# Kernel tuning notes

Measured on AMD Instinct MI355X. Metric: run time of the kernel, lower is better.

The kernel has to match this reference:

```python
import jax, jax.numpy as jnp
import numpy as np


def setup_inputs() -> dict:
    key = jax.random.key(0)
    bs, n_heads, ch, length = 4, 8, 64, 2048
    width = 3 * n_heads * ch  # 1536
    qkv = jax.random.normal(key, (bs, width, length), dtype=jnp.float32)
    return {"qkv": qkv, "n_heads": n_heads}


def reference(qkv, n_heads):
    bs, width, length = qkv.shape
    ch = width // (3 * n_heads)
    # reshape to (bs*heads, 3*ch, length) then split into q, k, v of (B, ch, L)
    qkv_r = qkv.reshape(bs * n_heads, 3 * ch, length)
    q, k, v = qkv_r[:, :ch], qkv_r[:, ch:2 * ch], qkv_r[:, 2 * ch:]
    scale = ch ** (-0.5)
    # weight = bmm(q^T, k) * scale -> (B, L_q, L_k)
    weight = jnp.einsum('bct,bcs->bts', q, k) * scale
    weight = jax.nn.softmax(weight.astype(jnp.float32), axis=-1).astype(qkv.dtype)
    # a = bmm(v, weight^T) -> (B, ch, L)
    a = jnp.einsum('bcs,bts->bct', v, weight)
    return a.reshape(bs, n_heads * ch, length)
```

## Files before the change

### kernel.cpp

```cpp
#include <hip/hip_runtime.h>

typedef __bf16 bf16;
typedef __attribute__((ext_vector_type(8)))  __bf16 bf16x8;
typedef __attribute__((ext_vector_type(16))) float  f32x16;

#define LEN   2048
#define CH    64
#define HEADS 32

union PackU { unsigned u[4]; bf16x8 v; };

static __device__ inline unsigned pack2(float lo, float hi) {
  union { bf16 h[2]; unsigned u; } p;
  p.h[0] = (bf16)lo; p.h[1] = (bf16)hi;
  return p.u;
}

static __device__ inline void async_cp16(const bf16* g, bf16* l) {
  __builtin_amdgcn_global_load_lds(
      (const __attribute__((address_space(1))) void*)g,
      (__attribute__((address_space(3))) void*)l, 16, 0, 0);
}

__global__ __launch_bounds__(256) void prep_kernel(const float* __restrict__ qkv,
                                                   bf16* __restrict__ ws) {
  __shared__ float tile[64][65];
  const int tIdx = blockIdx.x;
  const int g    = blockIdx.y;
  const int tid  = threadIdx.x;
  const int s0   = tIdx * 64;
  const float* K = qkv + (g * 192 + 64)  * LEN;
  const float* V = qkv + (g * 192 + 128) * LEN;

  {
    const int c0 = tid >> 6, s = tid & 63;
#pragma unroll
    for (int i = 0; i < 16; ++i) {
      const int c = c0 + i * 4;
      tile[c][s] = K[c * LEN + s0 + s];
    }
  }
  __syncthreads();

  bf16* dst = ws + ((size_t)g * 32 + tIdx) * 8192;
#pragma unroll
  for (int it = 0; it < 2; ++it) {
    const int c2  = tid + it * 256;
    const int row = c2 >> 3, cx = c2 & 7;
    const int cb  = (cx ^ (row & 7)) * 8;
    bf16x8 o;
#pragma unroll
    for (int j = 0; j < 8; ++j) o[j] = (bf16)tile[cb + j][row];
    *(bf16x8*)(dst + c2 * 8) = o;
  }
#pragma unroll
  for (int it = 0; it < 2; ++it) {
    const int c2  = tid + it * 256;
    const int row = c2 >> 3, cx = c2 & 7;
    const int k8  = cx ^ (row & 7);
    const int pa  = 32 * (k8 >> 2) + 8 * ((k8 >> 1) & 1) + 4 * (k8 & 1);
    const float* src = V + row * LEN + s0 + pa;
    const float4 a = *(const float4*)src;
    const float4 b = *(const float4*)(src + 16);
    bf16x8 o;
    o[0] = (bf16)a.x; o[1] = (bf16)a.y; o[2] = (bf16)a.z; o[3] = (bf16)a.w;
    o[4] = (bf16)b.x; o[5] = (bf16)b.y; o[6] = (bf16)b.z; o[7] = (bf16)b.w;
    *(bf16x8*)(dst + 4096 + c2 * 8) = o;
  }
}

__global__ __launch_bounds__(512, 2) void attn_kernel(const float* __restrict__ qkv,
                                                      const bf16* __restrict__ ws,
                                                      float* __restrict__ out) {
  __shared__ __align__(16) bf16 stg[32768];

  const int tid  = threadIdx.x;
  const int lane = tid & 63;
  const int w    = tid >> 6;
  const int wg   = w & 3;
  const int sg   = w >> 2;
  const int n    = lane & 31;
  const int h    = lane >> 5;
  const int g    = blockIdx.x & 31;
  const int jb   = blockIdx.x >> 5;
  const int t0   = jb * 256 + wg * 64;

  const bf16* wsg = ws + (size_t)g * (32 * 8192);

  auto stage = [&](int i) {
    const bf16* src = wsg + i * 8192;
    bf16* dst = stg + (i & 3) * 8192;
#pragma unroll
    for (int it = 0; it < 2; ++it) {
      const int chunk = w * 128 + it * 64 + lane;
      async_cp16(src + chunk * 8, dst + chunk * 8);
    }
  };
  stage(0); stage(1);

  const float qs = 0.125f * 1.44269504088896340736f;
  const float* Q = qkv + g * (192 * LEN);
  bf16x8 qf[2][4];
#pragma unroll
  for (int e = 0; e < 2; ++e)
#pragma unroll
    for (int kb = 0; kb < 4; ++kb)
#pragma unroll
      for (int jj = 0; jj < 8; ++jj)
        qf[e][kb][jj] = (bf16)(Q[(kb * 16 + h * 8 + jj) * LEN + t0 + e * 32 + n] * qs);

  f32x16 o_acc[2][2];
#pragma unroll
  for (int e = 0; e < 2; ++e)
#pragma unroll
    for (int mb = 0; mb < 2; ++mb)
#pragma unroll
      for (int r = 0; r < 16; ++r) o_acc[e][mb][r] = 0.f;
  float l_acc[2] = {0.f, 0.f};

  for (int p = 0; p < 16; ++p) {
    __syncthreads();
    if (p < 15) { stage(2 * p + 2); stage(2 * p + 3); }
    const bf16* ktl = stg + ((2 * p + sg) & 3) * 8192;
    const bf16* vl  = ktl + 4096;

    f32x16 sf[2][2];
#pragma unroll
    for (int e = 0; e < 2; ++e)
#pragma unroll
      for (int mb = 0; mb < 2; ++mb)
#pragma unroll
        for (int r = 0; r < 16; ++r) sf[e][mb][r] = 0.f;
#pragma unroll
    for (int kb = 0; kb < 4; ++kb)
#pragma unroll
      for (int mb = 0; mb < 2; ++mb) {
        const bf16x8 a = *(const bf16x8*)(ktl + (mb * 32 + n) * 64 + (((kb * 2 + h) ^ (n & 7)) * 8));
        sf[0][mb] = __builtin_amdgcn_mfma_f32_32x32x16_bf16(a, qf[0][kb], sf[0][mb], 0, 0, 0);
        sf[1][mb] = __builtin_amdgcn_mfma_f32_32x32x16_bf16(a, qf[1][kb], sf[1][mb], 0, 0, 0);
      }

    PackU frag[2][4];
#pragma unroll
    for (int e = 0; e < 2; ++e) {
      float ls = 0.f;
#pragma unroll
      for (int mb = 0; mb < 2; ++mb)
#pragma unroll
        for (int u = 0; u < 4; ++u) {
          const float p0 = __builtin_amdgcn_exp2f(sf[e][mb][4 * u + 0]);
          const float p1 = __builtin_amdgcn_exp2f(sf[e][mb][4 * u + 1]);
          const float p2 = __builtin_amdgcn_exp2f(sf[e][mb][4 * u + 2]);
          const float p3 = __builtin_amdgcn_exp2f(sf[e][mb][4 * u + 3]);
          ls += (p0 + p1) + (p2 + p3);
          const int kb   = 2 * mb + (u & 1);
          const int base = 2 * (u >> 1);
          frag[e][kb].u[base]     = pack2(p0, p1);
          frag[e][kb].u[base + 1] = pack2(p2, p3);
        }
      l_acc[e] += ls;
    }

#pragma unroll
    for (int kbs = 0; kbs < 4; ++kbs)
#pragma unroll
      for (int mbo = 0; mbo < 2; ++mbo) {
        const bf16x8 a = *(const bf16x8*)(vl + (mbo * 32 + n) * 64 + (((kbs * 2 + h) ^ (n & 7)) * 8));
        o_acc[0][mbo] = __builtin_amdgcn_mfma_f32_32x32x16_bf16(a, frag[0][kbs].v, o_acc[0][mbo], 0, 0, 0);
        o_acc[1][mbo] = __builtin_amdgcn_mfma_f32_32x32x16_bf16(a, frag[1][kbs].v, o_acc[1][mbo], 0, 0, 0);
      }
  }

  float lt[2];
#pragma unroll
  for (int e = 0; e < 2; ++e) lt[e] = l_acc[e] + __shfl_xor(l_acc[e], 32);

  float* fx = (float*)stg;
  float* lx = fx + 15104;

#pragma unroll
  for (int mbo = 0; mbo < 2; ++mbo) {
    __syncthreads();
    if (sg == 1) {
#pragma unroll
      for (int e = 0; e < 2; ++e)
#pragma unroll
        for (int u = 0; u < 4; ++u) {
          float4 st;
          st.x = o_acc[e][mbo][4 * u + 0];
          st.y = o_acc[e][mbo][4 * u + 1];
          st.z = o_acc[e][mbo][4 * u + 2];
          st.w = o_acc[e][mbo][4 * u + 3];
          *(float4*)&fx[wg * 2304 + (e * 32 + n) * 36 + 8 * u + 4 * h] = st;
        }
      if (mbo == 0 && h == 0) {
        lx[wg * 64 + n]      = lt[0];
        lx[wg * 64 + 32 + n] = lt[1];
      }
    }
    __syncthreads();
    if (sg == 0) {
#pragma unroll
      for (int e = 0; e < 2; ++e)
#pragma unroll
        for (int u = 0; u < 4; ++u) {
          const float4 q = *(const float4*)&fx[wg * 2304 + (e * 32 + n) * 36 + 8 * u + 4 * h];
          o_acc[e][mbo][4 * u + 0] += q.x;
          o_acc[e][mbo][4 * u + 1] += q.y;
          o_acc[e][mbo][4 * u + 2] += q.z;
          o_acc[e][mbo][4 * u + 3] += q.w;
        }
    }
  }

  if (sg == 0) {
    float inv[2];
#pragma unroll
    for (int e = 0; e < 2; ++e) inv[e] = 1.0f / (lt[e] + lx[wg * 64 + e * 32 + n]);
    float* og = out + g * (CH * LEN);
#pragma unroll
    for (int e = 0; e < 2; ++e)
#pragma unroll
      for (int mbo = 0; mbo < 2; ++mbo)
#pragma unroll
        for (int r = 0; r < 16; ++r) {
          const int c = 32 * mbo + (r & 3) + 8 * (r >> 2) + 4 * h;
          og[c * LEN + t0 + e * 32 + n] = o_acc[e][mbo][r] * inv[e];
        }
  }
}

extern "C" void kernel_launch(void* const* d_in, const int* in_sizes, int n_in,
                              void* d_out, int out_size, void* d_ws, size_t ws_size,
                              hipStream_t stream) {
  const float* qkv = (const float*)d_in[0];
  float* out = (float*)d_out;
  bf16* ws = (bf16*)d_ws;

  prep_kernel<<<dim3(32, HEADS), 256, 0, stream>>>(qkv, ws);
  attn_kernel<<<dim3(256), 512, 0, stream>>>(qkv, ws, out);
}
```

Baseline: 127.5 us.

## Halve per-wave query tile, double grid, and add extra LDS swizzle term

Each wave now handles one 32-column query group instead of two. The workgroup covers 128 queries instead of 256, so the grid doubles to 512 blocks and launch bounds are raised to allow 4 blocks per CU. A second XOR term on the row's upper bits is added to the K/V LDS swizzle, in both the prep kernel and the attention reads, to reduce bank conflicts. The intent is more parallelism and occupancy from fewer accumulator registers. In exchange, each block reloads the full K/V stream for fewer queries, doubling K/V staging traffic per query, and each 64 KB LDS buffer may cap residency below the requested count.

```diff
diff --git a/kernel.cpp b/kernel.cpp
--- a/kernel.cpp
+++ b/kernel.cpp
@@ -47,7 +47,8 @@
   for (int it = 0; it < 2; ++it) {
     const int c2  = tid + it * 256;
     const int row = c2 >> 3, cx = c2 & 7;
-    const int cb  = (cx ^ (row & 7)) * 8;
+    const int k8  = cx ^ (row & 7) ^ ((row >> 3) & 7);
+    const int cb  = k8 * 8;
     bf16x8 o;
 #pragma unroll
     for (int j = 0; j < 8; ++j) o[j] = (bf16)tile[cb + j][row];
@@ -57,7 +58,7 @@
   for (int it = 0; it < 2; ++it) {
     const int c2  = tid + it * 256;
     const int row = c2 >> 3, cx = c2 & 7;
-    const int k8  = cx ^ (row & 7);
+    const int k8  = cx ^ (row & 7) ^ ((row >> 3) & 7);
     const int pa  = 32 * (k8 >> 2) + 8 * ((k8 >> 1) & 1) + 4 * (k8 & 1);
     const float* src = V + row * LEN + s0 + pa;
     const float4 a = *(const float4*)src;
@@ -69,7 +70,7 @@
   }
 }
 
-__global__ __launch_bounds__(512, 2) void attn_kernel(const float* __restrict__ qkv,
+__global__ __launch_bounds__(512, 4) void attn_kernel(const float* __restrict__ qkv,
                                                       const bf16* __restrict__ ws,
                                                       float* __restrict__ out) {
   __shared__ __align__(16) bf16 stg[32768];
@@ -77,13 +78,14 @@
   const int tid  = threadIdx.x;
   const int lane = tid & 63;
   const int w    = tid >> 6;
-  const int wg   = w & 3;
+  const int wg   = w & 1;
+  const int eg   = (w >> 1) & 1;
   const int sg   = w >> 2;
   const int n    = lane & 31;
   const int h    = lane >> 5;
   const int g    = blockIdx.x & 31;
   const int jb   = blockIdx.x >> 5;
-  const int t0   = jb * 256 + wg * 64;
+  const int t0   = jb * 128 + wg * 64;
 
   const bf16* wsg = ws + (size_t)g * (32 * 8192);
 
@@ -100,23 +102,19 @@
 
   const float qs = 0.125f * 1.44269504088896340736f;
   const float* Q = qkv + g * (192 * LEN);
-  bf16x8 qf[2][4];
-#pragma unroll
-  for (int e = 0; e < 2; ++e)
-#pragma unroll
-    for (int kb = 0; kb < 4; ++kb)
-#pragma unroll
-      for (int jj = 0; jj < 8; ++jj)
-        qf[e][kb][jj] = (bf16)(Q[(kb * 16 + h * 8 + jj) * LEN + t0 + e * 32 + n] * qs);
-
-  f32x16 o_acc[2][2];
-#pragma unroll
-  for (int e = 0; e < 2; ++e)
-#pragma unroll
-    for (int mb = 0; mb < 2; ++mb)
-#pragma unroll
-      for (int r = 0; r < 16; ++r) o_acc[e][mb][r] = 0.f;
-  float l_acc[2] = {0.f, 0.f};
+  bf16x8 qf[4];
+#pragma unroll
+  for (int kb = 0; kb < 4; ++kb)
+#pragma unroll
+    for (int jj = 0; jj < 8; ++jj)
+      qf[kb][jj] = (bf16)(Q[(kb * 16 + h * 8 + jj) * LEN + t0 + eg * 32 + n] * qs);
+
+  f32x16 o_acc[2];
+#pragma unroll
+  for (int mb = 0; mb < 2; ++mb)
+#pragma unroll
+    for (int r = 0; r < 16; ++r) o_acc[mb][r] = 0.f;
+  float l_acc = 0.f;
 
   for (int p = 0; p < 16; ++p) {
     __syncthreads();
@@ -124,109 +122,91 @@
     const bf16* ktl = stg + ((2 * p + sg) & 3) * 8192;
     const bf16* vl  = ktl + 4096;
 
-    f32x16 sf[2][2];
-#pragma unroll
-    for (int e = 0; e < 2; ++e)
-#pragma unroll
-      for (int mb = 0; mb < 2; ++mb)
-#pragma unroll
-        for (int r = 0; r < 16; ++r) sf[e][mb][r] = 0.f;
+    f32x16 sf[2];
+#pragma unroll
+    for (int mb = 0; mb < 2; ++mb)
+#pragma unroll
+      for (int r = 0; r < 16; ++r) sf[mb][r] = 0.f;
 #pragma unroll
     for (int kb = 0; kb < 4; ++kb)
 #pragma unroll
       for (int mb = 0; mb < 2; ++mb) {
-        const bf16x8 a = *(const bf16x8*)(ktl + (mb * 32 + n) * 64 + (((kb * 2 + h) ^ (n & 7)) * 8));
-        sf[0][mb] = __builtin_amdgcn_mfma_f32_32x32x16_bf16(a, qf[0][kb], sf[0][mb], 0, 0, 0);
-        sf[1][mb] = __builtin_amdgcn_mfma_f32_32x32x16_bf16(a, qf[1][kb], sf[1][mb], 0, 0, 0);
-      }
-
-    PackU frag[2][4];
-#pragma unroll
-    for (int e = 0; e < 2; ++e) {
-      float ls = 0.f;
-#pragma unroll
-      for (int mb = 0; mb < 2; ++mb)
-#pragma unroll
-        for (int u = 0; u < 4; ++u) {
-          const float p0 = __builtin_amdgcn_exp2f(sf[e][mb][4 * u + 0]);
-          const float p1 = __builtin_amdgcn_exp2f(sf[e][mb][4 * u + 1]);
-          const float p2 = __builtin_amdgcn_exp2f(sf[e][mb][4 * u + 2]);
-          const float p3 = __builtin_amdgcn_exp2f(sf[e][mb][4 * u + 3]);
-          ls += (p0 + p1) + (p2 + p3);
-          const int kb   = 2 * mb + (u & 1);
-          const int base = 2 * (u >> 1);
-          frag[e][kb].u[base]     = pack2(p0, p1);
-          frag[e][kb].u[base + 1] = pack2(p2, p3);
-        }
-      l_acc[e] += ls;
-    }
+        const bf16x8 a = *(const bf16x8*)(ktl + (mb * 32 + n) * 64 +
+                          (((kb * 2 + h) ^ (n & 7) ^ (mb << 2) ^ (n >> 3)) * 8));
+        sf[mb] = __builtin_amdgcn_mfma_f32_32x32x16_bf16(a, qf[kb], sf[mb], 0, 0, 0);
+      }
+
+    PackU frag[4];
+    float ls = 0.f;
+#pragma unroll
+    for (int mb = 0; mb < 2; ++mb)
+#pragma unroll
+      for (int u = 0; u < 4; ++u) {
+        const float p0 = __builtin_amdgcn_exp2f(sf[mb][4 * u + 0]);
+        const float p1 = __builtin_amdgcn_exp2f(sf[mb][4 * u + 1]);
+        const float p2 = __builtin_amdgcn_exp2f(sf[mb][4 * u + 2]);
+        const float p3 = __builtin_amdgcn_exp2f(sf[mb][4 * u + 3]);
+        ls += (p0 + p1) + (p2 + p3);
+        const int kb   = 2 * mb + (u & 1);
+        const int base = 2 * (u >> 1);
+        frag[kb].u[base]     = pack2(p0, p1);
+        frag[kb].u[base + 1] = pack2(p2, p3);
+      }
+    l_acc += ls;
 
 #pragma unroll
     for (int kbs = 0; kbs < 4; ++kbs)
 #pragma unroll
       for (int mbo = 0; mbo < 2; ++mbo) {
-        const bf16x8 a = *(const bf16x8*)(vl + (mbo * 32 + n) * 64 + (((kbs * 2 + h) ^ (n & 7)) * 8));
-        o_acc[0][mbo] = __builtin_amdgcn_mfma_f32_32x32x16_bf16(a, frag[0][kbs].v, o_acc[0][mbo], 0, 0, 0);
-        o_acc[1][mbo] = __builtin_amdgcn_mfma_f32_32x32x16_bf16(a, frag[1][kbs].v, o_acc[1][mbo], 0, 0, 0);
-      }
-  }
-
-  float lt[2];
-#pragma unroll
-  for (int e = 0; e < 2; ++e) lt[e] = l_acc[e] + __shfl_xor(l_acc[e], 32);
+        const bf16x8 a = *(const bf16x8*)(vl + (mbo * 32 + n) * 64 +
+                          (((kbs * 2 + h) ^ (n & 7) ^ (mbo << 2) ^ (n >> 3)) * 8));
+        o_acc[mbo] = __builtin_amdgcn_mfma_f32_32x32x16_bf16(a, frag[kbs].v, o_acc[mbo], 0, 0, 0);
+      }
+  }
+
+  float lt = l_acc + __shfl_xor(l_acc, 32);
 
   float* fx = (float*)stg;
-  float* lx = fx + 15104;
+  float* lx = fx + 4608;
 
 #pragma unroll
   for (int mbo = 0; mbo < 2; ++mbo) {
     __syncthreads();
     if (sg == 1) {
 #pragma unroll
-      for (int e = 0; e < 2; ++e)
-#pragma unroll
-        for (int u = 0; u < 4; ++u) {
-          float4 st;
-          st.x = o_acc[e][mbo][4 * u + 0];
-          st.y = o_acc[e][mbo][4 * u + 1];
-          st.z = o_acc[e][mbo][4 * u + 2];
-          st.w = o_acc[e][mbo][4 * u + 3];
-          *(float4*)&fx[wg * 2304 + (e * 32 + n) * 36 + 8 * u + 4 * h] = st;
-        }
-      if (mbo == 0 && h == 0) {
-        lx[wg * 64 + n]      = lt[0];
-        lx[wg * 64 + 32 + n] = lt[1];
-      }
+      for (int u = 0; u < 4; ++u) {
+        float4 st;
+        st.x = o_acc[mbo][4 * u + 0];
+        st.y = o_acc[mbo][4 * u + 1];
+        st.z = o_acc[mbo][4 * u + 2];
+        st.w = o_acc[mbo][4 * u + 3];
+        *(float4*)&fx[wg * 2304 + (eg * 32 + n) * 36 + 8 * u + 4 * h] = st;
+      }
+      if (mbo == 0 && h == 0) lx[wg * 64 + eg * 32 + n] = lt;
     }
     __syncthreads();
     if (sg == 0) {
 #pragma unroll
-      for (int e = 0; e < 2; ++e)
-#pragma unroll
-        for (int u = 0; u < 4; ++u) {
-          const float4 q = *(const float4*)&fx[wg * 2304 + (e * 32 + n) * 36 + 8 * u + 4 * h];
-          o_acc[e][mbo][4 * u + 0] += q.x;
-          o_acc[e][mbo][4 * u + 1] += q.y;
-          o_acc[e][mbo][4 * u + 2] += q.z;
-          o_acc[e][mbo][4 * u + 3] += q.w;
-        }
+      for (int u = 0; u < 4; ++u) {
+        const float4 q = *(const float4*)&fx[wg * 2304 + (eg * 32 + n) * 36 + 8 * u + 4 * h];
+        o_acc[mbo][4 * u + 0] += q.x;
+        o_acc[mbo][4 * u + 1] += q.y;
+        o_acc[mbo][4 * u + 2] += q.z;
+        o_acc[mbo][4 * u + 3] += q.w;
+      }
     }
   }
 
   if (sg == 0) {
-    float inv[2];
-#pragma unroll
-    for (int e = 0; e < 2; ++e) inv[e] = 1.0f / (lt[e] + lx[wg * 64 + e * 32 + n]);
+    const float inv = 1.0f / (lt + lx[wg * 64 + eg * 32 + n]);
     float* og = out + g * (CH * LEN);
 #pragma unroll
-    for (int e = 0; e < 2; ++e)
-#pragma unroll
-      for (int mbo = 0; mbo < 2; ++mbo)
-#pragma unroll
-        for (int r = 0; r < 16; ++r) {
-          const int c = 32 * mbo + (r & 3) + 8 * (r >> 2) + 4 * h;
-          og[c * LEN + t0 + e * 32 + n] = o_acc[e][mbo][r] * inv[e];
-        }
+    for (int mbo = 0; mbo < 2; ++mbo)
+#pragma unroll
+      for (int r = 0; r < 16; ++r) {
+        const int c = 32 * mbo + (r & 3) + 8 * (r >> 2) + 4 * h;
+        og[c * LEN + t0 + eg * 32 + n] = o_acc[mbo][r] * inv;
+      }
   }
 }
 
@@ -238,5 +218,5 @@
   bf16* ws = (bf16*)d_ws;
 
   prep_kernel<<<dim3(32, HEADS), 256, 0, stream>>>(qkv, ws);
-  attn_kernel<<<dim3(256), 512, 0, stream>>>(qkv, ws, out);
-}
+  attn_kernel<<<dim3(512), 512, 0, stream>>>(qkv, ws, out);
+}
```

After: 132.1 us. 3.6% more time.

## Software-pipeline QK/PV MFMAs with exp across query halves, reswizzle LDS layout

Applied to the files above, without the earlier changes.

The inner loop is split per query half so the exp/pack work for one half is interleaved with MFMAs for the other half. sched_group_barrier hints pair one MFMA with eight VALU ops in each group. All K and V fragments are preloaded from LDS at the start of each iteration. The swizzle in the prep kernel and in the LDS reads gains an extra XOR on the row-block bits to reduce bank conflicts. This adds register pressure from holding all the K and V fragments, which matters under launch_bounds(512,2).

```diff
diff --git a/kernel.cpp b/kernel.cpp
--- a/kernel.cpp
+++ b/kernel.cpp
@@ -47,7 +47,8 @@
   for (int it = 0; it < 2; ++it) {
     const int c2  = tid + it * 256;
     const int row = c2 >> 3, cx = c2 & 7;
-    const int cb  = (cx ^ (row & 7)) * 8;
+    const int k8  = cx ^ (row & 7) ^ ((row >> 3) & 7);
+    const int cb  = k8 * 8;
     bf16x8 o;
 #pragma unroll
     for (int j = 0; j < 8; ++j) o[j] = (bf16)tile[cb + j][row];
@@ -57,7 +58,7 @@
   for (int it = 0; it < 2; ++it) {
     const int c2  = tid + it * 256;
     const int row = c2 >> 3, cx = c2 & 7;
-    const int k8  = cx ^ (row & 7);
+    const int k8  = cx ^ (row & 7) ^ ((row >> 3) & 7);
     const int pa  = 32 * (k8 >> 2) + 8 * ((k8 >> 1) & 1) + 4 * (k8 & 1);
     const float* src = V + row * LEN + s0 + pa;
     const float4 a = *(const float4*)src;
@@ -124,51 +125,92 @@
     const bf16* ktl = stg + ((2 * p + sg) & 3) * 8192;
     const bf16* vl  = ktl + 4096;
 
-    f32x16 sf[2][2];
-#pragma unroll
-    for (int e = 0; e < 2; ++e)
-#pragma unroll
-      for (int mb = 0; mb < 2; ++mb)
-#pragma unroll
-        for (int r = 0; r < 16; ++r) sf[e][mb][r] = 0.f;
-#pragma unroll
-    for (int kb = 0; kb < 4; ++kb)
-#pragma unroll
-      for (int mb = 0; mb < 2; ++mb) {
-        const bf16x8 a = *(const bf16x8*)(ktl + (mb * 32 + n) * 64 + (((kb * 2 + h) ^ (n & 7)) * 8));
-        sf[0][mb] = __builtin_amdgcn_mfma_f32_32x32x16_bf16(a, qf[0][kb], sf[0][mb], 0, 0, 0);
-        sf[1][mb] = __builtin_amdgcn_mfma_f32_32x32x16_bf16(a, qf[1][kb], sf[1][mb], 0, 0, 0);
+    bf16x8 ka[4][2], vf[4][2];
+#pragma unroll
+    for (int kb = 0; kb < 4; ++kb)
+#pragma unroll
+      for (int mb = 0; mb < 2; ++mb)
+        ka[kb][mb] = *(const bf16x8*)(ktl + (mb * 32 + n) * 64 +
+                        (((kb * 2 + h) ^ (n & 7) ^ (mb << 2) ^ (n >> 3)) * 8));
+#pragma unroll
+    for (int kb = 0; kb < 4; ++kb)
+#pragma unroll
+      for (int mb = 0; mb < 2; ++mb)
+        vf[kb][mb] = *(const bf16x8*)(vl + (mb * 32 + n) * 64 +
+                        (((kb * 2 + h) ^ (n & 7) ^ (mb << 2) ^ (n >> 3)) * 8));
+
+    f32x16 sf0[2], sf1[2];
+#pragma unroll
+    for (int mb = 0; mb < 2; ++mb)
+#pragma unroll
+      for (int r = 0; r < 16; ++r) { sf0[mb][r] = 0.f; sf1[mb][r] = 0.f; }
+#pragma unroll
+    for (int kb = 0; kb < 4; ++kb)
+#pragma unroll
+      for (int mb = 0; mb < 2; ++mb)
+        sf0[mb] = __builtin_amdgcn_mfma_f32_32x32x16_bf16(ka[kb][mb], qf[0][kb], sf0[mb], 0, 0, 0);
+
+    PackU frag0[4];
+    float ls0 = 0.f;
+#pragma unroll
+    for (int kb = 0; kb < 4; ++kb)
+#pragma unroll
+      for (int mb = 0; mb < 2; ++mb)
+        sf1[mb] = __builtin_amdgcn_mfma_f32_32x32x16_bf16(ka[kb][mb], qf[1][kb], sf1[mb], 0, 0, 0);
+#pragma unroll
+    for (int mb = 0; mb < 2; ++mb)
+#pragma unroll
+      for (int u = 0; u < 4; ++u) {
+        const float p0 = __builtin_amdgcn_exp2f(sf0[mb][4 * u + 0]);
+        const float p1 = __builtin_amdgcn_exp2f(sf0[mb][4 * u + 1]);
+        const float p2 = __builtin_amdgcn_exp2f(sf0[mb][4 * u + 2]);
+        const float p3 = __builtin_amdgcn_exp2f(sf0[mb][4 * u + 3]);
+        ls0 += (p0 + p1) + (p2 + p3);
+        const int kb   = 2 * mb + (u & 1);
+        const int base = 2 * (u >> 1);
+        frag0[kb].u[base]     = pack2(p0, p1);
+        frag0[kb].u[base + 1] = pack2(p2, p3);
       }
-
-    PackU frag[2][4];
-#pragma unroll
-    for (int e = 0; e < 2; ++e) {
-      float ls = 0.f;
-#pragma unroll
-      for (int mb = 0; mb < 2; ++mb)
-#pragma unroll
-        for (int u = 0; u < 4; ++u) {
-          const float p0 = __builtin_amdgcn_exp2f(sf[e][mb][4 * u + 0]);
-          const float p1 = __builtin_amdgcn_exp2f(sf[e][mb][4 * u + 1]);
-          const float p2 = __builtin_amdgcn_exp2f(sf[e][mb][4 * u + 2]);
-          const float p3 = __builtin_amdgcn_exp2f(sf[e][mb][4 * u + 3]);
-          ls += (p0 + p1) + (p2 + p3);
-          const int kb   = 2 * mb + (u & 1);
-          const int base = 2 * (u >> 1);
-          frag[e][kb].u[base]     = pack2(p0, p1);
-          frag[e][kb].u[base + 1] = pack2(p2, p3);
-        }
-      l_acc[e] += ls;
-    }
-
+    l_acc[0] += ls0;
+#pragma unroll
+    for (int i = 0; i < 8; ++i) {
+      __builtin_amdgcn_sched_group_barrier(0x008, 1, 0);
+      __builtin_amdgcn_sched_group_barrier(0x002, 8, 0);
+    }
+
+    PackU frag1[4];
+    float ls1 = 0.f;
 #pragma unroll
     for (int kbs = 0; kbs < 4; ++kbs)
 #pragma unroll
-      for (int mbo = 0; mbo < 2; ++mbo) {
-        const bf16x8 a = *(const bf16x8*)(vl + (mbo * 32 + n) * 64 + (((kbs * 2 + h) ^ (n & 7)) * 8));
-        o_acc[0][mbo] = __builtin_amdgcn_mfma_f32_32x32x16_bf16(a, frag[0][kbs].v, o_acc[0][mbo], 0, 0, 0);
-        o_acc[1][mbo] = __builtin_amdgcn_mfma_f32_32x32x16_bf16(a, frag[1][kbs].v, o_acc[1][mbo], 0, 0, 0);
+      for (int mbo = 0; mbo < 2; ++mbo)
+        o_acc[0][mbo] = __builtin_amdgcn_mfma_f32_32x32x16_bf16(vf[kbs][mbo], frag0[kbs].v, o_acc[0][mbo], 0, 0, 0);
+#pragma unroll
+    for (int mb = 0; mb < 2; ++mb)
+#pragma unroll
+      for (int u = 0; u < 4; ++u) {
+        const float p0 = __builtin_amdgcn_exp2f(sf1[mb][4 * u + 0]);
+        const float p1 = __builtin_amdgcn_exp2f(sf1[mb][4 * u + 1]);
+        const float p2 = __builtin_amdgcn_exp2f(sf1[mb][4 * u + 2]);
+        const float p3 = __builtin_amdgcn_exp2f(sf1[mb][4 * u + 3]);
+        ls1 += (p0 + p1) + (p2 + p3);
+        const int kb   = 2 * mb + (u & 1);
+        const int base = 2 * (u >> 1);
+        frag1[kb].u[base]     = pack2(p0, p1);
+        frag1[kb].u[base + 1] = pack2(p2, p3);
       }
+    l_acc[1] += ls1;
+#pragma unroll
+    for (int i = 0; i < 8; ++i) {
+      __builtin_amdgcn_sched_group_barrier(0x008, 1, 0);
+      __builtin_amdgcn_sched_group_barrier(0x002, 8, 0);
+    }
+
+#pragma unroll
+    for (int kbs = 0; kbs < 4; ++kbs)
+#pragma unroll
+      for (int mbo = 0; mbo < 2; ++mbo)
+        o_acc[1][mbo] = __builtin_amdgcn_mfma_f32_32x32x16_bf16(vf[kbs][mbo], frag1[kbs].v, o_acc[1][mbo], 0, 0, 0);
   }
 
   float lt[2];
```

Result: no change. 125.7 us (-1.4%).

## Stagger wave-group schedules with 5-slot LDS ring and extra swizzle

Applied to the files above, without the earlier changes.

Moves the K/V ring buffer from 4 to 5 LDS slots, and each wave group now stages only its own tile. The second wave group runs a skewed software pipeline: it computes QK and softmax for the current tile but defers that tile's PV matmul to the next iteration. The intent is to keep the two groups out of phase so MFMA work from one overlaps exp/pack work from the other. The LDS XOR swizzle also gains row>>3 and mb terms to cut bank conflicts, and the QK accumulators start from a zero register. The cost is more LDS, which may reduce occupancy, plus more live registers for the carried fragments.

```diff
diff --git a/kernel.cpp b/kernel.cpp
--- a/kernel.cpp
+++ b/kernel.cpp
@@ -47,7 +47,8 @@
   for (int it = 0; it < 2; ++it) {
     const int c2  = tid + it * 256;
     const int row = c2 >> 3, cx = c2 & 7;
-    const int cb  = (cx ^ (row & 7)) * 8;
+    const int k8  = cx ^ (row & 7) ^ ((row >> 3) & 7);
+    const int cb  = k8 * 8;
     bf16x8 o;
 #pragma unroll
     for (int j = 0; j < 8; ++j) o[j] = (bf16)tile[cb + j][row];
@@ -57,7 +58,7 @@
   for (int it = 0; it < 2; ++it) {
     const int c2  = tid + it * 256;
     const int row = c2 >> 3, cx = c2 & 7;
-    const int k8  = cx ^ (row & 7);
+    const int k8  = cx ^ (row & 7) ^ ((row >> 3) & 7);
     const int pa  = 32 * (k8 >> 2) + 8 * ((k8 >> 1) & 1) + 4 * (k8 & 1);
     const float* src = V + row * LEN + s0 + pa;
     const float4 a = *(const float4*)src;
@@ -72,7 +73,7 @@
 __global__ __launch_bounds__(512, 2) void attn_kernel(const float* __restrict__ qkv,
                                                       const bf16* __restrict__ ws,
                                                       float* __restrict__ out) {
-  __shared__ __align__(16) bf16 stg[32768];
+  __shared__ __align__(16) bf16 stg[40960];
 
   const int tid  = threadIdx.x;
   const int lane = tid & 63;
@@ -87,16 +88,16 @@
 
   const bf16* wsg = ws + (size_t)g * (32 * 8192);
 
-  auto stage = [&](int i) {
+  auto stageH = [&](int i) {
     const bf16* src = wsg + i * 8192;
-    bf16* dst = stg + (i & 3) * 8192;
-#pragma unroll
-    for (int it = 0; it < 2; ++it) {
-      const int chunk = w * 128 + it * 64 + lane;
+    bf16* dst = stg + (i % 5) * 8192;
+#pragma unroll
+    for (int it = 0; it < 4; ++it) {
+      const int chunk = (w & 3) * 256 + it * 64 + lane;
       async_cp16(src + chunk * 8, dst + chunk * 8);
     }
   };
-  stage(0); stage(1);
+  if (sg == 0) stageH(0); else stageH(1);
 
   const float qs = 0.125f * 1.44269504088896340736f;
   const float* Q = qkv + g * (192 * LEN);
@@ -118,57 +119,99 @@
       for (int r = 0; r < 16; ++r) o_acc[e][mb][r] = 0.f;
   float l_acc[2] = {0.f, 0.f};
 
+  f32x16 zf;
+#pragma unroll
+  for (int r = 0; r < 16; ++r) zf[r] = 0.f;
+
+  PackU cfrag[2][4];
+
+  auto ldfr = [&](const bf16* basep, bf16x8 fr[4][2]) {
+#pragma unroll
+    for (int kb = 0; kb < 4; ++kb)
+#pragma unroll
+      for (int mb = 0; mb < 2; ++mb)
+        fr[kb][mb] = *(const bf16x8*)(basep + (mb * 32 + n) * 64 +
+                        (((kb * 2 + h) ^ (n & 7) ^ (mb << 2) ^ (n >> 3)) * 8));
+  };
+  auto qkmm = [&](const bf16x8 ka[4][2], const bf16x8* qe, f32x16* sf) {
+#pragma unroll
+    for (int mb = 0; mb < 2; ++mb)
+      sf[mb] = __builtin_amdgcn_mfma_f32_32x32x16_bf16(ka[0][mb], qe[0], zf, 0, 0, 0);
+#pragma unroll
+    for (int kb = 1; kb < 4; ++kb)
+#pragma unroll
+      for (int mb = 0; mb < 2; ++mb)
+        sf[mb] = __builtin_amdgcn_mfma_f32_32x32x16_bf16(ka[kb][mb], qe[kb], sf[mb], 0, 0, 0);
+  };
+  auto smax = [&](const f32x16* sf, PackU* fr, int e) {
+    float ls = 0.f;
+#pragma unroll
+    for (int mb = 0; mb < 2; ++mb)
+#pragma unroll
+      for (int u = 0; u < 4; ++u) {
+        const float p0 = __builtin_amdgcn_exp2f(sf[mb][4 * u + 0]);
+        const float p1 = __builtin_amdgcn_exp2f(sf[mb][4 * u + 1]);
+        const float p2 = __builtin_amdgcn_exp2f(sf[mb][4 * u + 2]);
+        const float p3 = __builtin_amdgcn_exp2f(sf[mb][4 * u + 3]);
+        ls += (p0 + p1) + (p2 + p3);
+        const int kb   = 2 * mb + (u & 1);
+        const int base = 2 * (u >> 1);
+        fr[kb].u[base]     = pack2(p0, p1);
+        fr[kb].u[base + 1] = pack2(p2, p3);
+      }
+    l_acc[e] += ls;
+  };
+  auto pvmm = [&](const bf16x8 vf[4][2], const PackU* fr, f32x16* oa) {
+#pragma unroll
+    for (int kbs = 0; kbs < 4; ++kbs)
+#pragma unroll
+      for (int mbo = 0; mbo < 2; ++mbo)
+        oa[mbo] = __builtin_amdgcn_mfma_f32_32x32x16_bf16(vf[kbs][mbo], fr[kbs].v, oa[mbo], 0, 0, 0);
+  };
+
   for (int p = 0; p < 16; ++p) {
     __syncthreads();
-    if (p < 15) { stage(2 * p + 2); stage(2 * p + 3); }
-    const bf16* ktl = stg + ((2 * p + sg) & 3) * 8192;
-    const bf16* vl  = ktl + 4096;
-
-    f32x16 sf[2][2];
-#pragma unroll
-    for (int e = 0; e < 2; ++e)
-#pragma unroll
-      for (int mb = 0; mb < 2; ++mb)
-#pragma unroll
-        for (int r = 0; r < 16; ++r) sf[e][mb][r] = 0.f;
-#pragma unroll
-    for (int kb = 0; kb < 4; ++kb)
-#pragma unroll
-      for (int mb = 0; mb < 2; ++mb) {
-        const bf16x8 a = *(const bf16x8*)(ktl + (mb * 32 + n) * 64 + (((kb * 2 + h) ^ (n & 7)) * 8));
-        sf[0][mb] = __builtin_amdgcn_mfma_f32_32x32x16_bf16(a, qf[0][kb], sf[0][mb], 0, 0, 0);
-        sf[1][mb] = __builtin_amdgcn_mfma_f32_32x32x16_bf16(a, qf[1][kb], sf[1][mb], 0, 0, 0);
+    if (sg == 0) {
+      if (p < 15) stageH(2 * p + 2);
+      const bf16* ktl = stg + ((2 * p) % 5) * 8192;
+      const bf16* vl  = ktl + 4096;
+      bf16x8 ka[4][2];
+      ldfr(ktl, ka);
+      f32x16 sf0[2], sf1[2];
+      qkmm(ka, qf[0], sf0);
+      qkmm(ka, qf[1], sf1);
+      bf16x8 vf[4][2];
+      ldfr(vl, vf);
+      PackU fr0[4], fr1[4];
+      smax(sf0, fr0, 0);
+      pvmm(vf, fr0, o_acc[0]);
+      smax(sf1, fr1, 1);
+      pvmm(vf, fr1, o_acc[1]);
+    } else {
+      if (p > 0) {
+        const bf16* vp = stg + ((2 * p + 4) % 5) * 8192 + 4096;
+        bf16x8 vf[4][2];
+        ldfr(vp, vf);
+        pvmm(vf, cfrag[0], o_acc[0]);
+        pvmm(vf, cfrag[1], o_acc[1]);
       }
-
-    PackU frag[2][4];
-#pragma unroll
-    for (int e = 0; e < 2; ++e) {
-      float ls = 0.f;
-#pragma unroll
-      for (int mb = 0; mb < 2; ++mb)
-#pragma unroll
-        for (int u = 0; u < 4; ++u) {
-          const float p0 = __builtin_amdgcn_exp2f(sf[e][mb][4 * u + 0]);
-          const float p1 = __builtin_amdgcn_exp2f(sf[e][mb][4 * u + 1]);
-          const float p2 = __builtin_amdgcn_exp2f(sf[e][mb][4 * u + 2]);
-          const float p3 = __builtin_amdgcn_exp2f(sf[e][mb][4 * u + 3]);
-          ls += (p0 + p1) + (p2 + p3);
-          const int kb   = 2 * mb + (u & 1);
-          const int base = 2 * (u >> 1);
-          frag[e][kb].u[base]     = pack2(p0, p1);
-          frag[e][kb].u[base + 1] = pack2(p2, p3);
-        }
-      l_acc[e] += ls;
-    }
-
-#pragma unroll
-    for (int kbs = 0; kbs < 4; ++kbs)
-#pragma unroll
-      for (int mbo = 0; mbo < 2; ++mbo) {
-        const bf16x8 a = *(const bf16x8*)(vl + (mbo * 32 + n) * 64 + (((kbs * 2 + h) ^ (n & 7)) * 8));
-        o_acc[0][mbo] = __builtin_amdgcn_mfma_f32_32x32x16_bf16(a, frag[0][kbs].v, o_acc[0][mbo], 0, 0, 0);
-        o_acc[1][mbo] = __builtin_amdgcn_mfma_f32_32x32x16_bf16(a, frag[1][kbs].v, o_acc[1][mbo], 0, 0, 0);
-      }
+      if (p < 15) stageH(2 * p + 3);
+      const bf16* ktl = stg + ((2 * p + 1) % 5) * 8192;
+      bf16x8 ka[4][2];
+      ldfr(ktl, ka);
+      f32x16 sf0[2], sf1[2];
+      qkmm(ka, qf[0], sf0);
+      qkmm(ka, qf[1], sf1);
+      smax(sf0, cfrag[0], 0);
+      smax(sf1, cfrag[1], 1);
+    }
+  }
+  if (sg == 1) {
+    const bf16* vp = stg + (31 % 5) * 8192 + 4096;
+    bf16x8 vf[4][2];
+    ldfr(vp, vf);
+    pvmm(vf, cfrag[0], o_acc[0]);
+    pvmm(vf, cfrag[1], o_acc[1]);
   }
 
   float lt[2];
```

After: 144.1 us. 13.0% more time.
